# Optimization experiments

Hardware: AMD Instinct MI355X
Metric: run time of the kernel (lower is better)

Reference implementation:

```python
import jax, jax.numpy as jnp
import numpy as np

# KronLinear config (input_dim=output_dim=4096, factorized as 64x64, rank=4)
A1, A2 = 64, 64   # a_shape = [input_dims[0], output_dims[1]]
B1, B2 = 64, 64   # b_shape = [input_dims[1], output_dims[0]]
RANK = 4


def setup_inputs() -> dict:
    key = jax.random.key(0)
    kx, ka, kb, kbias = jax.random.split(key, 4)
    x = jax.random.normal(kx, (4, 2048, 4096), dtype=jnp.float32)
    # xavier_uniform over last two dims of (rank, d1, d2)
    lim_a = float(np.sqrt(6.0 / (A1 + A2)))
    lim_b = float(np.sqrt(6.0 / (B1 + B2)))
    A = jax.random.uniform(ka, (RANK, A1, A2), minval=-lim_a, maxval=lim_a, dtype=jnp.float32)
    B = jax.random.uniform(kb, (RANK, B1, B2), minval=-lim_b, maxval=lim_b, dtype=jnp.float32)
    bias = jax.random.normal(kbias, (A2 * B2,), dtype=jnp.float32)
    return {"x": x, "A": A, "B": B, "bias": bias}


def reference(x, A, B, bias):
    # Faithful translation of KronLinear.forward, including the torch .view
    # that reinterprets the flattened (b2, rank) axis as (rank, b2).
    x_shape = x.shape
    xf = x.reshape(-1, A1, B1)                              # (N, a1, b1)
    Bf = jnp.transpose(B, (1, 2, 0)).reshape(B1, B2 * RANK)  # (b1, b2*rank)
    t = jnp.einsum('nab,bc->nac', xf, Bf)                    # (N, a1, b2*rank)
    t = t.reshape(-1, A1, RANK, B2)                          # reinterpret as (rank, b2)!
    t = jnp.transpose(t, (2, 0, 3, 1)).reshape(RANK, -1, A1) # (rank, N*b2, a1)
    o = jnp.einsum('rna,rac->rnc', t, A)                     # bmm -> (rank, N*b2, a2)
    o = o.sum(axis=0)                                        # (N*b2, a2)
    o = o.reshape(-1, B2, A2)                                # (N, b2, a2)
    o = jnp.swapaxes(o, 1, 2).reshape(-1, A2 * B2)           # (N, a2*b2)
    out = o.reshape(x_shape[:-1] + (A2 * B2,)) + bias
    return out
```

## Files before the change

kernel.cpp:

```cpp
#include <hip/hip_runtime.h>


typedef __attribute__((ext_vector_type(8))) short bf16x8;
typedef __attribute__((ext_vector_type(4))) float f32x4;

__device__ __forceinline__ unsigned short f2bf(float f) {
    unsigned int u = __builtin_bit_cast(unsigned int, f);
    unsigned int r = u + 0x7fffu + ((u >> 16) & 1u);
    return (unsigned short)(r >> 16);
}

__global__ __launch_bounds__(256) void kron_prep(const float* __restrict__ A,
                                                 const float* __restrict__ B,
                                                 unsigned short* __restrict__ ws)
{
    int f = blockIdx.x * 256 + threadIdx.x;
    if (f < 16384) {
        int e = f & 7, l = (f >> 3) & 63, ks = (f >> 9) & 1, ct = f >> 10;
        int b1 = ks * 32 + (l >> 4) * 8 + e;
        int c  = ct * 16 + (l & 15);
        int bb = c & 63, rr = c >> 6;
        float v = B[(bb & 3) * 4096 + b1 * 64 + (rr * 16 + (bb >> 2))];
        ws[f] = f2bf(v);
    } else {
        int f2 = f - 16384;
        int e = f2 & 7, l = (f2 >> 3) & 63, ks = (f2 >> 9) & 7, at = f2 >> 12;
        int k = ks * 32 + (l >> 4) * 8 + e;
        int rr = k >> 6, a1 = k & 63;
        int a2 = at * 16 + (l & 15);
        float v = A[rr * 4096 + a1 * 64 + a2];
        ws[16384 + f2] = f2bf(v);
    }
}

__global__ __launch_bounds__(256, 2) void kron_main(const float* __restrict__ x,
                                                    const float* __restrict__ bias,
                                                    const unsigned short* __restrict__ ws,
                                                    float* __restrict__ out)
{
    __shared__ unsigned short Xs[64 * 64];
    __shared__ unsigned short Ts[256 * 64];

    const int n = blockIdx.x;
    const float* __restrict__ xp = x + (size_t)n * 4096;
    float* __restrict__ op = out + (size_t)n * 4096;

    const int t  = threadIdx.x;
    const int w  = t >> 6;
    const int l  = t & 63;
    const int lr = l & 15;
    const int lg = l >> 4;

    #pragma unroll
    for (int it = 0; it < 4; ++it) {
        int idx = it * 1024 + t * 4;
        float4 v = *reinterpret_cast<const float4*>(xp + idx);
        int a1 = idx >> 6, b1 = idx & 63;
        unsigned int p0 = (unsigned int)f2bf(v.x) | ((unsigned int)f2bf(v.y) << 16);
        unsigned int p1 = (unsigned int)f2bf(v.z) | ((unsigned int)f2bf(v.w) << 16);
        int colb = (b1 * 2) ^ ((a1 & 7) << 4);
        *reinterpret_cast<uint2*>(reinterpret_cast<char*>(Xs) + a1 * 128 + colb) =
            make_uint2(p0, p1);
    }
    __syncthreads();

    f32x4 acc[4][4];
    #pragma unroll
    for (int i = 0; i < 4; ++i)
        #pragma unroll
        for (int j = 0; j < 4; ++j)
            acc[i][j] = (f32x4){0.f, 0.f, 0.f, 0.f};

    const unsigned short* __restrict__ Bq = ws;
    #pragma unroll
    for (int ks = 0; ks < 2; ++ks) {
        bf16x8 bfrag[4];
        #pragma unroll
        for (int ci = 0; ci < 4; ++ci) {
            int ct = w * 4 + ci;
            bfrag[ci] = *reinterpret_cast<const bf16x8*>(Bq + ((ct * 2 + ks) * 64 + l) * 8);
        }
        #pragma unroll
        for (int a1t = 0; a1t < 4; ++a1t) {
            int row  = a1t * 16 + lr;
            int colb = ((ks * 32 + lg * 8) * 2) ^ ((row & 7) << 4);
            bf16x8 afrag = *reinterpret_cast<const bf16x8*>(
                reinterpret_cast<const char*>(Xs) + row * 128 + colb);
            #pragma unroll
            for (int ci = 0; ci < 4; ++ci)
                acc[a1t][ci] = __builtin_amdgcn_mfma_f32_16x16x32_bf16(
                    afrag, bfrag[ci], acc[a1t][ci], 0, 0, 0);
        }
    }

    #pragma unroll
    for (int a1t = 0; a1t < 4; ++a1t) {
        #pragma unroll
        for (int ci = 0; ci < 4; ++ci) {
            int ct   = w * 4 + ci;
            int crow = ct * 16 + lr;
            int a1c  = a1t * 16 + lg * 4;
            f32x4 d = acc[a1t][ci];
            unsigned int p0 = (unsigned int)f2bf(d[0]) | ((unsigned int)f2bf(d[1]) << 16);
            unsigned int p1 = (unsigned int)f2bf(d[2]) | ((unsigned int)f2bf(d[3]) << 16);
            int colb = (a1c * 2) ^ ((crow & 7) << 4);
            *reinterpret_cast<uint2*>(reinterpret_cast<char*>(Ts) + crow * 128 + colb) =
                make_uint2(p0, p1);
        }
    }
    __syncthreads();

    f32x4 acc2[4];
    #pragma unroll
    for (int j = 0; j < 4; ++j) acc2[j] = (f32x4){0.f, 0.f, 0.f, 0.f};

    const unsigned short* __restrict__ Af = ws + 16384;
    #pragma unroll
    for (int ks = 0; ks < 8; ++ks) {
        bf16x8 bop = *reinterpret_cast<const bf16x8*>(Af + ((w * 8 + ks) * 64 + l) * 8);
        #pragma unroll
        for (int bt = 0; bt < 4; ++bt) {
            int crow = (ks >> 1) * 64 + bt * 16 + lr;
            int a1c  = (ks & 1) * 32 + lg * 8;
            int colb = (a1c * 2) ^ ((crow & 7) << 4);
            bf16x8 aop = *reinterpret_cast<const bf16x8*>(
                reinterpret_cast<const char*>(Ts) + crow * 128 + colb);
            acc2[bt] = __builtin_amdgcn_mfma_f32_16x16x32_bf16(aop, bop, acc2[bt], 0, 0, 0);
        }
    }

    #pragma unroll
    for (int bt = 0; bt < 4; ++bt) {
        int a2  = w * 16 + lr;
        int b2  = bt * 16 + lg * 4;
        int idx = a2 * 64 + b2;
        float4 bv = *reinterpret_cast<const float4*>(bias + idx);
        f32x4 d = acc2[bt];
        float4 o = make_float4(d[0] + bv.x, d[1] + bv.y, d[2] + bv.z, d[3] + bv.w);
        *reinterpret_cast<float4*>(op + idx) = o;
    }
}

extern "C" void kernel_launch(void* const* d_in, const int* in_sizes, int n_in,
                              void* d_out, int out_size, void* d_ws, size_t ws_size,
                              hipStream_t stream) {
    const float* x    = (const float*)d_in[0];
    const float* A    = (const float*)d_in[1];
    const float* B    = (const float*)d_in[2];
    const float* bias = (const float*)d_in[3];
    float* out = (float*)d_out;
    unsigned short* ws = (unsigned short*)d_ws;

    kron_prep<<<128, 256, 0, stream>>>(A, B, ws);
    kron_main<<<8192, 256, 0, stream>>>(x, bias, ws, out);
}
```

Measured before the change: 244.9 us.

## Process four tiles per block with register prefetch and per-wave second GEMM

Each block now handles four consecutive rows of x instead of one, prefetching the next tile's x into registers while the second GEMM runs. The first GEMM is split into two halves to cut register pressure. Intermediate results are laid out per wave so each wave does the second GEMM on its own b2 slice, and launch bounds are raised for higher occupancy. Output uses nontemporal stores. The aim is to hide global load latency and amortize launch and setup cost, at the price of fewer blocks and extra loop-carried registers.

Result: slower. 619.9 us (+153.1%).

```diff
diff --git a/kernel.cpp b/kernel.cpp
--- a/kernel.cpp
+++ b/kernel.cpp
@@ -33,17 +33,15 @@
     }
 }
 
-__global__ __launch_bounds__(256, 2) void kron_main(const float* __restrict__ x,
+#define TPB_TILES 4
+
+__global__ __launch_bounds__(256, 4) void kron_main(const float* __restrict__ x,
                                                     const float* __restrict__ bias,
                                                     const unsigned short* __restrict__ ws,
                                                     float* __restrict__ out)
 {
     __shared__ unsigned short Xs[64 * 64];
-    __shared__ unsigned short Ts[256 * 64];
-
-    const int n = blockIdx.x;
-    const float* __restrict__ xp = x + (size_t)n * 4096;
-    float* __restrict__ op = out + (size_t)n * 4096;
+    __shared__ unsigned short Tw[4 * 16 * 256];
 
     const int t  = threadIdx.x;
     const int w  = t >> 6;
@@ -51,93 +49,110 @@
     const int lr = l & 15;
     const int lg = l >> 4;
 
-    #pragma unroll
-    for (int it = 0; it < 4; ++it) {
-        int idx = it * 1024 + t * 4;
-        float4 v = *reinterpret_cast<const float4*>(xp + idx);
-        int a1 = idx >> 6, b1 = idx & 63;
-        unsigned int p0 = (unsigned int)f2bf(v.x) | ((unsigned int)f2bf(v.y) << 16);
-        unsigned int p1 = (unsigned int)f2bf(v.z) | ((unsigned int)f2bf(v.w) << 16);
-        int colb = (b1 * 2) ^ ((a1 & 7) << 4);
-        *reinterpret_cast<uint2*>(reinterpret_cast<char*>(Xs) + a1 * 128 + colb) =
-            make_uint2(p0, p1);
-    }
-    __syncthreads();
+    const unsigned short* __restrict__ Bq = ws;
+    const unsigned short* __restrict__ Af = ws + 16384;
 
-    f32x4 acc[4][4];
-    #pragma unroll
-    for (int i = 0; i < 4; ++i)
+    const size_t tile0 = (size_t)blockIdx.x * TPB_TILES;
+
+    f32x4 pf[4];
+    {
+        const float* __restrict__ xp = x + tile0 * 4096;
         #pragma unroll
-        for (int j = 0; j < 4; ++j)
-            acc[i][j] = (f32x4){0.f, 0.f, 0.f, 0.f};
-
-    const unsigned short* __restrict__ Bq = ws;
-    #pragma unroll
-    for (int ks = 0; ks < 2; ++ks) {
-        bf16x8 bfrag[4];
-        #pragma unroll
-        for (int ci = 0; ci < 4; ++ci) {
-            int ct = w * 4 + ci;
-            bfrag[ci] = *reinterpret_cast<const bf16x8*>(Bq + ((ct * 2 + ks) * 64 + l) * 8);
-        }
-        #pragma unroll
-        for (int a1t = 0; a1t < 4; ++a1t) {
-            int row  = a1t * 16 + lr;
-            int colb = ((ks * 32 + lg * 8) * 2) ^ ((row & 7) << 4);
-            bf16x8 afrag = *reinterpret_cast<const bf16x8*>(
-                reinterpret_cast<const char*>(Xs) + row * 128 + colb);
-            #pragma unroll
-            for (int ci = 0; ci < 4; ++ci)
-                acc[a1t][ci] = __builtin_amdgcn_mfma_f32_16x16x32_bf16(
-                    afrag, bfrag[ci], acc[a1t][ci], 0, 0, 0);
-        }
+        for (int it = 0; it < 4; ++it)
+            pf[it] = *reinterpret_cast<const f32x4*>(xp + it * 1024 + t * 4);
     }
 
-    #pragma unroll
-    for (int a1t = 0; a1t < 4; ++a1t) {
+    for (int tt = 0; tt < TPB_TILES; ++tt) {
         #pragma unroll
-        for (int ci = 0; ci < 4; ++ci) {
-            int ct   = w * 4 + ci;
-            int crow = ct * 16 + lr;
-            int a1c  = a1t * 16 + lg * 4;
-            f32x4 d = acc[a1t][ci];
-            unsigned int p0 = (unsigned int)f2bf(d[0]) | ((unsigned int)f2bf(d[1]) << 16);
-            unsigned int p1 = (unsigned int)f2bf(d[2]) | ((unsigned int)f2bf(d[3]) << 16);
-            int colb = (a1c * 2) ^ ((crow & 7) << 4);
-            *reinterpret_cast<uint2*>(reinterpret_cast<char*>(Ts) + crow * 128 + colb) =
+        for (int it = 0; it < 4; ++it) {
+            int idx = it * 1024 + t * 4;
+            int a1 = idx >> 6, b1 = idx & 63;
+            f32x4 v = pf[it];
+            unsigned int p0 = (unsigned int)f2bf(v[0]) | ((unsigned int)f2bf(v[1]) << 16);
+            unsigned int p1 = (unsigned int)f2bf(v[2]) | ((unsigned int)f2bf(v[3]) << 16);
+            int colb = (b1 * 2) ^ ((a1 & 7) << 4);
+            *reinterpret_cast<uint2*>(reinterpret_cast<char*>(Xs) + a1 * 128 + colb) =
                 make_uint2(p0, p1);
         }
-    }
-    __syncthreads();
+        __syncthreads();
 
-    f32x4 acc2[4];
-    #pragma unroll
-    for (int j = 0; j < 4; ++j) acc2[j] = (f32x4){0.f, 0.f, 0.f, 0.f};
+        #pragma unroll
+        for (int h = 0; h < 2; ++h) {
+            f32x4 acc1[2][4];
+            #pragma unroll
+            for (int cj = 0; cj < 2; ++cj)
+                #pragma unroll
+                for (int a1t = 0; a1t < 4; ++a1t)
+                    acc1[cj][a1t] = (f32x4){0.f, 0.f, 0.f, 0.f};
 
-    const unsigned short* __restrict__ Af = ws + 16384;
-    #pragma unroll
-    for (int ks = 0; ks < 8; ++ks) {
-        bf16x8 bop = *reinterpret_cast<const bf16x8*>(Af + ((w * 8 + ks) * 64 + l) * 8);
+            #pragma unroll
+            for (int ks = 0; ks < 2; ++ks) {
+                bf16x8 bfr[2];
+                #pragma unroll
+                for (int cj = 0; cj < 2; ++cj) {
+                    int ct = (2 * h + cj) * 4 + w;
+                    bfr[cj] = *reinterpret_cast<const bf16x8*>(Bq + ((ct * 2 + ks) * 64 + l) * 8);
+                }
+                #pragma unroll
+                for (int a1t = 0; a1t < 4; ++a1t) {
+                    int row  = a1t * 16 + lr;
+                    int colb = ((ks * 32 + lg * 8) * 2) ^ ((row & 7) << 4);
+                    bf16x8 af = *reinterpret_cast<const bf16x8*>(
+                        reinterpret_cast<const char*>(Xs) + row * 128 + colb);
+                    acc1[0][a1t] = __builtin_amdgcn_mfma_f32_16x16x32_bf16(af, bfr[0], acc1[0][a1t], 0, 0, 0);
+                    acc1[1][a1t] = __builtin_amdgcn_mfma_f32_16x16x32_bf16(af, bfr[1], acc1[1][a1t], 0, 0, 0);
+                }
+            }
+            #pragma unroll
+            for (int cj = 0; cj < 2; ++cj) {
+                #pragma unroll
+                for (int a1t = 0; a1t < 4; ++a1t) {
+                    int ci = 2 * h + cj;
+                    int k0 = ci * 64 + a1t * 16 + lg * 4;
+                    f32x4 d = acc1[cj][a1t];
+                    unsigned int p0 = (unsigned int)f2bf(d[0]) | ((unsigned int)f2bf(d[1]) << 16);
+                    unsigned int p1 = (unsigned int)f2bf(d[2]) | ((unsigned int)f2bf(d[3]) << 16);
+                    int colb = (k0 * 2) ^ ((lr & 7) << 4);
+                    *reinterpret_cast<uint2*>(reinterpret_cast<char*>(Tw)
+                        + w * 8192 + lr * 512 + colb) = make_uint2(p0, p1);
+                }
+            }
+        }
+        __syncthreads();
+
+        if (tt + 1 < TPB_TILES) {
+            const float* __restrict__ xp = x + (tile0 + tt + 1) * 4096;
+            #pragma unroll
+            for (int it = 0; it < 4; ++it)
+                pf[it] = *reinterpret_cast<const f32x4*>(xp + it * 1024 + t * 4);
+        }
+
+        f32x4 acc2[4];
         #pragma unroll
-        for (int bt = 0; bt < 4; ++bt) {
-            int crow = (ks >> 1) * 64 + bt * 16 + lr;
-            int a1c  = (ks & 1) * 32 + lg * 8;
-            int colb = (a1c * 2) ^ ((crow & 7) << 4);
+        for (int at = 0; at < 4; ++at) acc2[at] = (f32x4){0.f, 0.f, 0.f, 0.f};
+
+        #pragma unroll
+        for (int ks8 = 0; ks8 < 8; ++ks8) {
+            int colb = (ks8 * 64 + lg * 16) ^ ((lr & 7) << 4);
             bf16x8 aop = *reinterpret_cast<const bf16x8*>(
-                reinterpret_cast<const char*>(Ts) + crow * 128 + colb);
-            acc2[bt] = __builtin_amdgcn_mfma_f32_16x16x32_bf16(aop, bop, acc2[bt], 0, 0, 0);
+                reinterpret_cast<const char*>(Tw) + w * 8192 + lr * 512 + colb);
+            #pragma unroll
+            for (int at = 0; at < 4; ++at) {
+                bf16x8 bop = *reinterpret_cast<const bf16x8*>(Af + ((at * 8 + ks8) * 64 + l) * 8);
+                acc2[at] = __builtin_amdgcn_mfma_f32_16x16x32_bf16(aop, bop, acc2[at], 0, 0, 0);
+            }
         }
-    }
 
-    #pragma unroll
-    for (int bt = 0; bt < 4; ++bt) {
-        int a2  = w * 16 + lr;
-        int b2  = bt * 16 + lg * 4;
-        int idx = a2 * 64 + b2;
-        float4 bv = *reinterpret_cast<const float4*>(bias + idx);
-        f32x4 d = acc2[bt];
-        float4 o = make_float4(d[0] + bv.x, d[1] + bv.y, d[2] + bv.z, d[3] + bv.w);
-        *reinterpret_cast<float4*>(op + idx) = o;
+        float* __restrict__ op = out + (tile0 + tt) * 4096;
+        const int ob = 16 * w + lg * 4;
+        #pragma unroll
+        for (int at = 0; at < 4; ++at) {
+            int idx = (at * 16 + lr) * 64 + ob;
+            f32x4 bv = *reinterpret_cast<const f32x4*>(bias + idx);
+            f32x4 d = acc2[at];
+            f32x4 o = d + bv;
+            __builtin_nontemporal_store(o, reinterpret_cast<f32x4*>(op + idx));
+        }
     }
 }
 
@@ -152,5 +167,5 @@
     unsigned short* ws = (unsigned short*)d_ws;
 
     kron_prep<<<128, 256, 0, stream>>>(A, B, ws);
-    kron_main<<<8192, 256, 0, stream>>>(x, bias, ws, out);
+    kron_main<<<8192 / TPB_TILES, 256, 0, stream>>>(x, bias, ws, out);
 }
```
